# Optimization experiments

Measured on AMD Instinct MI355X. Metric: run time of the kernel, lower is better.

The kernel has to match this reference:

```python
import jax, jax.numpy as jnp
import numpy as np

BN_EPS = 1e-5
K = 3  # k_size


def _unfold(x, k):
    # torch F.unfold with padding=k//2, stride=1, viewed as (B, C, k*k, H, W).
    # Kernel positions are row-major (i slow, j fast), matching torch layout.
    p = k // 2
    B, C, H, W = x.shape
    xp = jnp.pad(x, ((0, 0), (0, 0), (p, p), (p, p)))
    pats = jnp.stack([xp[:, :, i:i + H, j:j + W]
                      for i in range(k) for j in range(k)], axis=2)
    return pats  # (B, C, k*k, H, W)


def _conv1x1(x, w, b):
    # w: (C_out, C_in), x: (B, C_in, H, W)
    return jnp.einsum('oc,bchw->bohw', w, x) + b[None, :, None, None]


def _bn(x, gamma, beta, mean, var):
    inv = gamma / jnp.sqrt(var + BN_EPS)
    return x * inv[None, :, None, None] + (beta - mean * inv)[None, :, None, None]


def setup_inputs() -> dict:
    key = jax.random.key(0)
    ks = jax.random.split(key, 12)
    B, C, H, W = 8, 256, 64, 64
    s = lambda k_, *sh: jax.random.normal(k_, sh, dtype=jnp.float32) * 0.05
    return {
        'x': jax.random.normal(ks[0], (B, C, H, W), dtype=jnp.float32),
        # feature_embedding: Conv2d(C, C, 1) + BN
        'w_embed': s(ks[1], C, C), 'b_embed': jnp.zeros((C,), jnp.float32),
        'bn1_gamma': jnp.ones((C,), jnp.float32), 'bn1_beta': jnp.zeros((C,), jnp.float32),
        'bn1_mean': jnp.zeros((C,), jnp.float32), 'bn1_var': jnp.ones((C,), jnp.float32),
        # enhance: Conv2d(2C, C, 1) + BN
        'w_enh': s(ks[2], C, 2 * C), 'b_enh': jnp.zeros((C,), jnp.float32),
        'bn2_gamma': jnp.ones((C,), jnp.float32), 'bn2_beta': jnp.zeros((C,), jnp.float32),
        'bn2_mean': jnp.zeros((C,), jnp.float32), 'bn2_var': jnp.ones((C,), jnp.float32),
        # weight_gen: Conv2d(2C, C//4, 1) -> ReLU -> Conv2d(C//4, C, 1) -> Sigmoid
        'w_g1': s(ks[3], C // 4, 2 * C), 'b_g1': jnp.zeros((C // 4,), jnp.float32),
        'w_g2': s(ks[4], C, C // 4), 'b_g2': jnp.zeros((C,), jnp.float32),
    }


def reference(x, w_embed, b_embed, bn1_gamma, bn1_beta, bn1_mean, bn1_var,
              w_enh, b_enh, bn2_gamma, bn2_beta, bn2_mean, bn2_var,
              w_g1, b_g1, w_g2, b_g2):
    B, C, H, W = x.shape
    # ---- feature embedding: 1x1 conv + BN (eval) + ReLU
    fe = jax.nn.relu(_bn(_conv1x1(x, w_embed, b_embed),
                         bn1_gamma, bn1_beta, bn1_mean, bn1_var))
    # ---- region similarity: cosine(center pixel, each kxk neighbor) over C
    pats = _unfold(fe, K)                       # (B, C, k2, H, W)
    sim = jnp.einsum('bchw,bckhw->bkhw', fe, pats)
    norm_c = jnp.sqrt(jnp.sum(fe * fe, axis=1))             # (B, H, W)
    norm_p = jnp.sqrt(jnp.sum(pats * pats, axis=1))         # (B, k2, H, W)
    sim = sim / (norm_c[:, None] * norm_p + 1e-7)
    sim = jax.nn.softmax(sim, axis=1)                       # over k2 window
    # ---- dynamic feature aggregation on original x
    xpats = _unfold(x, K)                                   # (B, C, k2, H, W)
    agg = jnp.einsum('bckhw,bkhw->bchw', xpats, sim)
    enhanced = jax.nn.relu(_bn(_conv1x1(jnp.concatenate([x, agg], axis=1), w_enh, b_enh),
                               bn2_gamma, bn2_beta, bn2_mean, bn2_var))
    # ---- output modulation (SE-style gating)
    pooled = jnp.mean(jnp.concatenate([x, enhanced], axis=1), axis=(2, 3), keepdims=True)
    h = jax.nn.relu(_conv1x1(pooled, w_g1, b_g1))
    weights = jax.nn.sigmoid(_conv1x1(h, w_g2, b_g2))       # (B, C, 1, 1)
    return x + weights * enhanced
```

## Files before the change

### kernel.cpp

```cpp
#include <hip/hip_runtime.h>
#include <math.h>

typedef unsigned short u16;
typedef unsigned int   u32;
typedef __attribute__((ext_vector_type(8))) short short8;
typedef __attribute__((ext_vector_type(4))) float f32x4;

#define HW 4096

#define OFS_XB   0ul
#define OFS_PD   8388608ul
#define OFS_W1B  8683520ul
#define OFS_W2B  8716288ul
#define OFS_B1   8781824ul
#define OFS_B2   8782080ul
#define OFS_POOL 8782336ul
#define OFS_GATE 8786432ul

__device__ __forceinline__ u16 f2bf(float x) {
    union { float f; u32 u; } v; v.f = x;
    u32 r = v.u + 0x7fffu + ((v.u >> 16) & 1u);
    return (u16)(r >> 16);
}
__device__ __forceinline__ float bf2f(u16 h) {
    union { u32 u; float f; } v; v.u = ((u32)h) << 16;
    return v.f;
}
__device__ __forceinline__ void ld_g2l_16(u16* l, const u16* g) {
    __builtin_amdgcn_global_load_lds(
        (const __attribute__((address_space(1))) u32*)g,
        (__attribute__((address_space(3))) u32*)l,
        16, 0, 0);
}

__global__ __launch_bounds__(256) void k_prep(
    const float* __restrict__ w1, const float* __restrict__ b1,
    const float* __restrict__ g1, const float* __restrict__ be1,
    const float* __restrict__ m1, const float* __restrict__ v1,
    const float* __restrict__ w2, const float* __restrict__ b2,
    const float* __restrict__ g2, const float* __restrict__ be2,
    const float* __restrict__ m2, const float* __restrict__ v2,
    u16* __restrict__ w1b, u16* __restrict__ w2b,
    float* __restrict__ b1f, float* __restrict__ b2f)
{
    int idx = blockIdx.x * 256 + threadIdx.x;
    if (idx < 65536) {
        int o = idx >> 8;
        float inv = g1[o] * rsqrtf(v1[o] + 1e-5f);
        w1b[idx] = f2bf(w1[idx] * inv);
    } else if (idx < 196608) {
        int j = idx - 65536;
        int o = j >> 9;
        float inv = g2[o] * rsqrtf(v2[o] + 1e-5f);
        w2b[j] = f2bf(w2[j] * inv);
    } else if (idx < 196864) {
        int o = idx - 196608;
        float inv = g1[o] * rsqrtf(v1[o] + 1e-5f);
        b1f[o] = b1[o] * inv + be1[o] - m1[o] * inv;
    } else if (idx < 197120) {
        int o = idx - 196864;
        float inv = g2[o] * rsqrtf(v2[o] + 1e-5f);
        b2f[o] = b2[o] * inv + be2[o] - m2[o] * inv;
    }
}

__global__ __launch_bounds__(256) void k_cvt(
    const float* __restrict__ x, u16* __restrict__ xb)
{
    __shared__ float tile[64][65];
    const int t = threadIdx.x;
    const int id = blockIdx.x;
    const int pt = id & 63, ct = (id >> 6) & 3, b = id >> 8;
    const float* src = x + (((size_t)(b * 256 + ct * 64)) << 12) + pt * 64;
#pragma unroll
    for (int i = 0; i < 16; ++i) {
        int idx = i * 256 + t;
        int cl = idx >> 6, pl = idx & 63;
        tile[cl][pl] = src[((size_t)cl << 12) + pl];
    }
    __syncthreads();
#pragma unroll
    for (int i = 0; i < 8; ++i) {
        int idx = i * 256 + t;
        int pl = idx >> 5, c2 = idx & 31;
        int cl = c2 * 2;
        u32 lo = f2bf(tile[cl][pl]);
        u32 hi = f2bf(tile[cl + 1][pl]);
        u32 pv = lo | (hi << 16);
        *(u32*)(xb + (((size_t)(b * 4096 + pt * 64 + pl)) << 9) + ct * 64 + cl) = pv;
    }
}

template<int KIN, bool OUTBF>
__global__ __launch_bounds__(256) void k_gemm(
    const u16* __restrict__ xb, const u16* __restrict__ Wb,
    const float* __restrict__ biasf, void* __restrict__ outp)
{
    __shared__ __align__(16) u16 Wl[4096];
    __shared__ __align__(16) u16 Xl[4096];
    __shared__ float sbias[128];
    const int t = threadIdx.x;
    const int lane = t & 63;
    const int wv = t >> 6;
    const int p_blk = blockIdx.x * 128;
    const int o_blk = blockIdx.y * 128;
    const int owg = (wv & 1) * 4;
    const int pwg = (wv >> 1) * 4;
    const int r16 = lane & 15, q = lane >> 4;
    if (t < 128) sbias[t] = biasf[o_blk + t];

    f32x4 acc[4][4];
#pragma unroll
    for (int i = 0; i < 4; ++i)
#pragma unroll
        for (int j = 0; j < 4; ++j) acc[i][j] = (f32x4){0.f, 0.f, 0.f, 0.f};

    for (int kc = 0; kc < KIN / 32; ++kc) {
        const int kk = kc * 32 + q * 8;
#pragma unroll
        for (int s = 0; s < 4; ++s) {
            const int bi = wv * 4 + s;
            const u16* g;
            u16* l;
            if (bi < 8) {
                g = Wb + (size_t)(o_blk + bi * 16 + r16) * KIN + kk;
                l = Wl + bi * 512;
            } else {
                g = xb + (((size_t)(p_blk + (bi - 8) * 16 + r16)) << 9) + kk;
                l = Xl + (bi - 8) * 512;
            }
            ld_g2l_16(l, g);
        }
        __syncthreads();
        short8 af[4], bf[4];
#pragma unroll
        for (int i = 0; i < 4; ++i) af[i] = *(const short8*)(Wl + (owg + i) * 512 + lane * 8);
#pragma unroll
        for (int j = 0; j < 4; ++j) bf[j] = *(const short8*)(Xl + (pwg + j) * 512 + lane * 8);
#pragma unroll
        for (int i = 0; i < 4; ++i)
#pragma unroll
            for (int j = 0; j < 4; ++j)
                acc[i][j] = __builtin_amdgcn_mfma_f32_16x16x32_bf16(af[i], bf[j], acc[i][j], 0, 0, 0);
        __syncthreads();
    }

    float bia[4][4];
#pragma unroll
    for (int i = 0; i < 4; ++i)
#pragma unroll
        for (int r = 0; r < 4; ++r) bia[i][r] = sbias[owg * 16 + i * 16 + q * 4 + r];
    const int bidx = p_blk >> 12;
    const int pin0 = (p_blk & 4095) + pwg * 16 + r16;
#pragma unroll
    for (int i = 0; i < 4; ++i) {
#pragma unroll
        for (int r = 0; r < 4; ++r) {
            const int o = o_blk + owg * 16 + i * 16 + q * 4 + r;
            const size_t rowb = ((size_t)(bidx * 256 + o)) << 12;
#pragma unroll
            for (int j = 0; j < 4; ++j) {
                float v = fmaxf(acc[i][j][r] + bia[i][r], 0.f);
                const size_t oi = rowb + pin0 + j * 16;
                if (OUTBF) ((u16*)outp)[oi] = f2bf(v);
                else       ((float*)outp)[oi] = v;
            }
        }
    }
}

__global__ __launch_bounds__(256) void k_sim(
    const u16* __restrict__ fe, float* __restrict__ pd)
{
    __shared__ __align__(16) u16 st[3 * 4096];
    __shared__ float red[4][64][9];
    const int t = threadIdx.x;
    const int id = blockIdx.x;
    const int g = id & 3, h = (id >> 2) & 63, b = id >> 8;
    const int rows[3] = {h > 0 ? h - 1 : 0, h, h < 63 ? h + 1 : 63};
    const u16* base = fe + (((size_t)(b * 256 + g * 64)) << 12);
#pragma unroll
    for (int it = 0; it < 6; ++it) {
        const int flat = it * 256 + t;
        const int r = flat >> 9, j = flat & 511;
        const u16* gs = base + ((size_t)(j >> 3) << 12) + rows[r] * 64 + (j & 7) * 8;
        ld_g2l_16(st + r * 4096 + j * 8, gs);
    }
    __syncthreads();
    const int w = t & 63, sl = t >> 6;
    const int wl = w > 0 ? w - 1 : 0, wr = w < 63 ? w + 1 : 63;
    float dot[9] = {};
    const u16* s0 = st + sl * 16 * 64;
#pragma unroll 4
    for (int ci = 0; ci < 16; ++ci) {
        const u16* pc = s0 + ci * 64;
        float v[9];
#pragma unroll
        for (int r = 0; r < 3; ++r) {
            v[r * 3 + 0] = bf2f(pc[r * 4096 + wl]);
            v[r * 3 + 1] = bf2f(pc[r * 4096 + w]);
            v[r * 3 + 2] = bf2f(pc[r * 4096 + wr]);
        }
        const float c0 = v[4];
#pragma unroll
        for (int k = 0; k < 9; ++k) dot[k] = fmaf(c0, v[k], dot[k]);
    }
#pragma unroll
    for (int k = 0; k < 9; ++k) red[sl][w][k] = dot[k];
    __syncthreads();
    if (t < 64) {
        const int p = h * 64 + w;
#pragma unroll
        for (int k = 0; k < 9; ++k) {
            float s = red[0][w][k] + red[1][w][k] + red[2][w][k] + red[3][w][k];
            atomicAdd(&pd[((size_t)(b * 9 + k) << 12) + p], s);
        }
    }
}

__global__ __launch_bounds__(256) void k_agg(
    const u16* __restrict__ xb, const float* __restrict__ pd,
    u16* __restrict__ xbo)
{
    __shared__ __align__(16) u16 xt[3 * 4096];
    __shared__ float ws9[9][64];
    const int t = threadIdx.x;
    const int id = blockIdx.x;
    const int g = id & 3, h = (id >> 2) & 63, b = id >> 8;
    const int rows[3] = {h > 0 ? h - 1 : 0, h, h < 63 ? h + 1 : 63};
    const u16* base = xb + (((size_t)(b * 4096)) << 9) + g * 64;
#pragma unroll
    for (int it = 0; it < 6; ++it) {
        const int flat = it * 256 + t;
        const int r = flat >> 9, j = flat & 511;
        const u16* gs = base + (((size_t)(rows[r] * 64 + (j >> 3))) << 9) + (j & 7) * 8;
        ld_g2l_16(xt + r * 4096 + j * 8, gs);
    }
    if (t < 64) {
        const int w = t;
        const int p = h * 64 + w;
        const float* pb = pd + (((size_t)(b * 9)) << 12);
        const float nc = sqrtf(pb[(4 << 12) + p]);
        float s[9], mk[9];
#pragma unroll
        for (int di = -1; di <= 1; ++di)
#pragma unroll
            for (int dj = -1; dj <= 1; ++dj) {
                const int k = (di + 1) * 3 + (dj + 1);
                const int hn = h + di, wn = w + dj;
                const float mask = (hn >= 0 && hn < 64 && wn >= 0 && wn < 64) ? 1.f : 0.f;
                const int hc = hn < 0 ? 0 : (hn > 63 ? 63 : hn);
                const int wc = wn < 0 ? 0 : (wn > 63 ? 63 : wn);
                const float nk = pb[(4 << 12) + hc * 64 + wc];
                const float dk = pb[(k << 12) + p];
                mk[k] = mask;
                s[k] = mask * dk / (nc * sqrtf(nk) + 1e-7f);
            }
        float mx = s[0];
#pragma unroll
        for (int k = 1; k < 9; ++k) mx = fmaxf(mx, s[k]);
        float e[9], sum = 0.f;
#pragma unroll
        for (int k = 0; k < 9; ++k) { e[k] = expf(s[k] - mx); sum += e[k]; }
        const float rs = 1.f / sum;
#pragma unroll
        for (int k = 0; k < 9; ++k) ws9[k][w] = mk[k] * e[k] * rs;
    }
    __syncthreads();
    const int c = t & 63, pg = t >> 6;
    u16* orow = xbo + (((size_t)(b * 4096 + h * 64)) << 9) + 256 + g * 64 + c;
#pragma unroll 4
    for (int pi = 0; pi < 16; ++pi) {
        const int px = pg * 16 + pi;
        const int pl = px > 0 ? px - 1 : 0, pr = px < 63 ? px + 1 : 63;
        const int pxs[3] = {pl, px, pr};
        float m[9];
#pragma unroll
        for (int k = 0; k < 9; ++k) m[k] = ws9[k][px];
        float acc = 0.f;
#pragma unroll
        for (int r = 0; r < 3; ++r)
#pragma unroll
            for (int j = 0; j < 3; ++j)
                acc = fmaf(bf2f(xt[r * 4096 + pxs[j] * 64 + c]), m[r * 3 + j], acc);
        orow[(size_t)px << 9] = f2bf(acc);
    }
}

__global__ __launch_bounds__(256) void k_pool(
    const float* __restrict__ x, const float* __restrict__ enh,
    float* __restrict__ pool)
{
    const int t = threadIdx.x;
    const int g = blockIdx.x * 4 + (t >> 6);
    const int lane = t & 63;
    const int b = g >> 9, j = g & 511;
    const float* src = (j < 256) ? x + (size_t)(b * 256 + j) * HW
                                 : enh + (size_t)(b * 256 + j - 256) * HW;
    float s = 0.f;
    for (int i = 0; i < 64; ++i) s += src[lane + i * 64];
    for (int off = 32; off > 0; off >>= 1) s += __shfl_down(s, off, 64);
    if (lane == 0) pool[g] = s * (1.f / 4096.f);
}

__global__ __launch_bounds__(64) void k_mlp(
    const float* __restrict__ pool,
    const float* __restrict__ wg1, const float* __restrict__ bg1,
    const float* __restrict__ wg2, const float* __restrict__ bg2,
    float* __restrict__ gate)
{
    __shared__ float pl[512];
    __shared__ float hb[64];
    const int b = blockIdx.x, t = threadIdx.x;
    for (int i = t; i < 512; i += 64) pl[i] = pool[b * 512 + i];
    __syncthreads();
    float s = bg1[t];
    const float* wr = wg1 + t * 512;
    for (int c = 0; c < 512; ++c) s = fmaf(wr[c], pl[c], s);
    hb[t] = fmaxf(s, 0.f);
    __syncthreads();
#pragma unroll
    for (int rr = 0; rr < 4; ++rr) {
        const int o = t + rr * 64;
        float s2 = bg2[o];
        const float* w2 = wg2 + o * 64;
        for (int j = 0; j < 64; ++j) s2 = fmaf(w2[j], hb[j], s2);
        gate[b * 256 + o] = 1.f / (1.f + expf(-s2));
    }
}

__global__ __launch_bounds__(256) void k_final(
    const float* __restrict__ x, const float* __restrict__ gate,
    float* __restrict__ out)
{
    const int idx = blockIdx.x * 256 + threadIdx.x;
    const int e = idx << 2;
    const int b = e >> 20;
    const int c = (e >> 12) & 255;
    const float g = gate[b * 256 + c];
    float4 xv = *(const float4*)(x + e);
    float4 ov = *(const float4*)(out + e);
    float4 rres;
    rres.x = fmaf(g, ov.x, xv.x);
    rres.y = fmaf(g, ov.y, xv.y);
    rres.z = fmaf(g, ov.z, xv.z);
    rres.w = fmaf(g, ov.w, xv.w);
    *(float4*)(out + e) = rres;
}

extern "C" void kernel_launch(void* const* d_in, const int* in_sizes, int n_in,
                              void* d_out, int out_size, void* d_ws, size_t ws_size,
                              hipStream_t stream)
{
    const float* x       = (const float*)d_in[0];
    const float* w_embed = (const float*)d_in[1];
    const float* b_embed = (const float*)d_in[2];
    const float* g1      = (const float*)d_in[3];
    const float* be1     = (const float*)d_in[4];
    const float* m1      = (const float*)d_in[5];
    const float* v1      = (const float*)d_in[6];
    const float* w_enh   = (const float*)d_in[7];
    const float* b_enh   = (const float*)d_in[8];
    const float* g2      = (const float*)d_in[9];
    const float* be2     = (const float*)d_in[10];
    const float* m2      = (const float*)d_in[11];
    const float* v2      = (const float*)d_in[12];
    const float* w_g1    = (const float*)d_in[13];
    const float* b_g1    = (const float*)d_in[14];
    const float* w_g2    = (const float*)d_in[15];
    const float* b_g2    = (const float*)d_in[16];
    float* ws  = (float*)d_ws;
    float* out = (float*)d_out;

    u16*   xb   = (u16*)(ws + OFS_XB);
    float* pd   = ws + OFS_PD;
    u16*   w1b  = (u16*)(ws + OFS_W1B);
    u16*   w2b  = (u16*)(ws + OFS_W2B);
    float* b1f  = ws + OFS_B1;
    float* b2f  = ws + OFS_B2;
    float* pool = ws + OFS_POOL;
    float* gate = ws + OFS_GATE;
    u16*   fe   = (u16*)d_out;

    hipMemsetAsync(pd, 0, (size_t)8 * 9 * 4096 * 4, stream);
    k_prep<<<dim3(770), dim3(256), 0, stream>>>(
        w_embed, b_embed, g1, be1, m1, v1,
        w_enh, b_enh, g2, be2, m2, v2, w1b, w2b, b1f, b2f);
    k_cvt<<<dim3(2048), dim3(256), 0, stream>>>(x, xb);
    k_gemm<256, true><<<dim3(256, 2), dim3(256), 0, stream>>>(xb, w1b, b1f, (void*)fe);
    k_sim<<<dim3(2048), dim3(256), 0, stream>>>(fe, pd);
    k_agg<<<dim3(2048), dim3(256), 0, stream>>>(xb, pd, xb);
    k_gemm<512, false><<<dim3(256, 2), dim3(256), 0, stream>>>(xb, w2b, b2f, (void*)out);
    k_pool<<<dim3(1024), dim3(256), 0, stream>>>(x, out, pool);
    k_mlp<<<dim3(8), dim3(64), 0, stream>>>(pool, w_g1, b_g1, w_g2, b_g2, gate);
    k_final<<<dim3(8192), dim3(256), 0, stream>>>(x, gate, out);
}
```

Baseline: 227.5 us.

## Fuse pooling into convert and GEMM epilogues, store enhanced as bf16

```diff
diff --git a/kernel.cpp b/kernel.cpp
--- a/kernel.cpp
+++ b/kernel.cpp
@@ -16,6 +16,7 @@
 #define OFS_B2   8782080ul
 #define OFS_POOL 8782336ul
 #define OFS_GATE 8786432ul
+#define OFS_ENH  8788480ul
 
 __device__ __forceinline__ u16 f2bf(float x) {
     union { float f; u32 u; } v; v.f = x;
@@ -41,9 +42,18 @@
     const float* __restrict__ g2, const float* __restrict__ be2,
     const float* __restrict__ m2, const float* __restrict__ v2,
     u16* __restrict__ w1b, u16* __restrict__ w2b,
-    float* __restrict__ b1f, float* __restrict__ b2f)
-{
-    int idx = blockIdx.x * 256 + threadIdx.x;
+    float* __restrict__ b1f, float* __restrict__ b2f,
+    float* __restrict__ pd, float* __restrict__ pool)
+{
+    const int bid = blockIdx.x, t = threadIdx.x;
+    if (bid >= 770) {
+        const int zid = bid - 770;
+        const float4 z = {0.f, 0.f, 0.f, 0.f};
+        if (zid < 288) ((float4*)(pd + zid * 1024))[t] = z;
+        else           ((float4*)(pool + (zid - 288) * 1024))[t] = z;
+        return;
+    }
+    int idx = bid * 256 + t;
     if (idx < 65536) {
         int o = idx >> 8;
         float inv = g1[o] * rsqrtf(v1[o] + 1e-5f);
@@ -65,7 +75,7 @@
 }
 
 __global__ __launch_bounds__(256) void k_cvt(
-    const float* __restrict__ x, u16* __restrict__ xb)
+    const float* __restrict__ x, u16* __restrict__ xb, float* __restrict__ pool)
 {
     __shared__ float tile[64][65];
     const int t = threadIdx.x;
@@ -89,12 +99,19 @@
         u32 pv = lo | (hi << 16);
         *(u32*)(xb + (((size_t)(b * 4096 + pt * 64 + pl)) << 9) + ct * 64 + cl) = pv;
     }
-}
-
-template<int KIN, bool OUTBF>
+    if (t < 64) {
+        float s = 0.f;
+#pragma unroll
+        for (int i = 0; i < 64; ++i) s += tile[t][i];
+        atomicAdd(&pool[(b << 9) + ct * 64 + t], s * (1.f / 4096.f));
+    }
+}
+
+template<int KIN, bool OUTBF, bool DOPOOL>
 __global__ __launch_bounds__(256) void k_gemm(
     const u16* __restrict__ xb, const u16* __restrict__ Wb,
-    const float* __restrict__ biasf, void* __restrict__ outp)
+    const float* __restrict__ biasf, void* __restrict__ outp,
+    float* __restrict__ poolp)
 {
     __shared__ __align__(16) u16 Wl[4096];
     __shared__ __align__(16) u16 Xl[4096];
@@ -158,12 +175,22 @@
         for (int r = 0; r < 4; ++r) {
             const int o = o_blk + owg * 16 + i * 16 + q * 4 + r;
             const size_t rowb = ((size_t)(bidx * 256 + o)) << 12;
+            float ps = 0.f;
 #pragma unroll
             for (int j = 0; j < 4; ++j) {
                 float v = fmaxf(acc[i][j][r] + bia[i][r], 0.f);
                 const size_t oi = rowb + pin0 + j * 16;
                 if (OUTBF) ((u16*)outp)[oi] = f2bf(v);
                 else       ((float*)outp)[oi] = v;
+                ps += v;
+            }
+            if (DOPOOL) {
+                ps += __shfl_down(ps, 8, 16);
+                ps += __shfl_down(ps, 4, 16);
+                ps += __shfl_down(ps, 2, 16);
+                ps += __shfl_down(ps, 1, 16);
+                if (r16 == 0)
+                    atomicAdd(&poolp[(bidx << 9) + 256 + o], ps * (1.f / 4096.f));
             }
         }
     }
@@ -287,22 +314,6 @@
     }
 }
 
-__global__ __launch_bounds__(256) void k_pool(
-    const float* __restrict__ x, const float* __restrict__ enh,
-    float* __restrict__ pool)
-{
-    const int t = threadIdx.x;
-    const int g = blockIdx.x * 4 + (t >> 6);
-    const int lane = t & 63;
-    const int b = g >> 9, j = g & 511;
-    const float* src = (j < 256) ? x + (size_t)(b * 256 + j) * HW
-                                 : enh + (size_t)(b * 256 + j - 256) * HW;
-    float s = 0.f;
-    for (int i = 0; i < 64; ++i) s += src[lane + i * 64];
-    for (int off = 32; off > 0; off >>= 1) s += __shfl_down(s, off, 64);
-    if (lane == 0) pool[g] = s * (1.f / 4096.f);
-}
-
 __global__ __launch_bounds__(64) void k_mlp(
     const float* __restrict__ pool,
     const float* __restrict__ wg1, const float* __restrict__ bg1,
@@ -330,8 +341,8 @@
 }
 
 __global__ __launch_bounds__(256) void k_final(
-    const float* __restrict__ x, const float* __restrict__ gate,
-    float* __restrict__ out)
+    const float* __restrict__ x, const u16* __restrict__ enh,
+    const float* __restrict__ gate, float* __restrict__ out)
 {
     const int idx = blockIdx.x * 256 + threadIdx.x;
     const int e = idx << 2;
@@ -339,12 +350,12 @@
     const int c = (e >> 12) & 255;
     const float g = gate[b * 256 + c];
     float4 xv = *(const float4*)(x + e);
-    float4 ov = *(const float4*)(out + e);
+    ushort4 ev = *(const ushort4*)(enh + e);
     float4 rres;
-    rres.x = fmaf(g, ov.x, xv.x);
-    rres.y = fmaf(g, ov.y, xv.y);
-    rres.z = fmaf(g, ov.z, xv.z);
-    rres.w = fmaf(g, ov.w, xv.w);
+    rres.x = fmaf(g, bf2f(ev.x), xv.x);
+    rres.y = fmaf(g, bf2f(ev.y), xv.y);
+    rres.z = fmaf(g, bf2f(ev.z), xv.z);
+    rres.w = fmaf(g, bf2f(ev.w), xv.w);
     *(float4*)(out + e) = rres;
 }
 
@@ -380,18 +391,17 @@
     float* b2f  = ws + OFS_B2;
     float* pool = ws + OFS_POOL;
     float* gate = ws + OFS_GATE;
+    u16*   enh  = (u16*)(ws + OFS_ENH);
     u16*   fe   = (u16*)d_out;
 
-    hipMemsetAsync(pd, 0, (size_t)8 * 9 * 4096 * 4, stream);
-    k_prep<<<dim3(770), dim3(256), 0, stream>>>(
+    k_prep<<<dim3(1062), dim3(256), 0, stream>>>(
         w_embed, b_embed, g1, be1, m1, v1,
-        w_enh, b_enh, g2, be2, m2, v2, w1b, w2b, b1f, b2f);
-    k_cvt<<<dim3(2048), dim3(256), 0, stream>>>(x, xb);
-    k_gemm<256, true><<<dim3(256, 2), dim3(256), 0, stream>>>(xb, w1b, b1f, (void*)fe);
+        w_enh, b_enh, g2, be2, m2, v2, w1b, w2b, b1f, b2f, pd, pool);
+    k_cvt<<<dim3(2048), dim3(256), 0, stream>>>(x, xb, pool);
+    k_gemm<256, true, false><<<dim3(256, 2), dim3(256), 0, stream>>>(xb, w1b, b1f, (void*)fe, nullptr);
     k_sim<<<dim3(2048), dim3(256), 0, stream>>>(fe, pd);
     k_agg<<<dim3(2048), dim3(256), 0, stream>>>(xb, pd, xb);
-    k_gemm<512, false><<<dim3(256, 2), dim3(256), 0, stream>>>(xb, w2b, b2f, (void*)out);
-    k_pool<<<dim3(1024), dim3(256), 0, stream>>>(x, out, pool);
+    k_gemm<512, true, true><<<dim3(256, 2), dim3(256), 0, stream>>>(xb, w2b, b2f, (void*)enh, pool);
     k_mlp<<<dim3(8), dim3(64), 0, stream>>>(pool, w_g1, b_g1, w_g2, b_g2, gate);
-    k_final<<<dim3(8192), dim3(256), 0, stream>>>(x, gate, out);
-}
+    k_final<<<dim3(8192), dim3(256), 0, stream>>>(x, enh, gate, out);
+}
```

Measured after the change: 214.6 us. -5.7%, faster.
